# Kernel tuning notes

Measured on AMD Instinct MI355X. Metric: run time of the kernel, lower is better.

The kernel has to match this reference:

```python
import jax, jax.numpy as jnp
import numpy as np

T, H, I = 8192, 4096, 11008  # tokens, hidden, intermediate (LLaMA-7B)


def setup_inputs() -> dict:
    key = jax.random.key(0)
    ks = jax.random.split(key, 8)
    # int8-valued tensors stored as int32 (spec dtype enum lacks int8)
    hidden_states = jax.random.randint(ks[0], (T, H), -128, 128, dtype=jnp.int32)
    gate_w = jax.random.randint(ks[1], (I, H), -128, 128, dtype=jnp.int32)
    up_w = jax.random.randint(ks[2], (I, H), -128, 128, dtype=jnp.int32)
    down_w = jax.random.randint(ks[3], (H, I), -128, 128, dtype=jnp.int32)
    # per-tensor dequant scales (alpha = input_scale * weight_scale); small so
    # the SwiGLU product lands roughly in int8 range before requantization
    gate_a = jnp.float32(0.004)
    up_a = jnp.float32(0.004)
    down_a = jnp.float32(0.004)
    gate_b = jax.random.normal(ks[4], (I,), dtype=jnp.float32)
    up_b = jax.random.normal(ks[5], (I,), dtype=jnp.float32)
    down_b = jax.random.normal(ks[6], (H,), dtype=jnp.float32)
    return dict(hidden_states=hidden_states, gate_w=gate_w, gate_a=gate_a,
                gate_b=gate_b, up_w=up_w, up_a=up_a, up_b=up_b,
                down_w=down_w, down_a=down_a, down_b=down_b)


def _w8a8_linear(x_i8, w_i8, alpha, bias):
    # scale alpha and fp32 bias (W8A8BFP32OFP32Linear semantics).
    acc = jnp.matmul(x_i8.astype(jnp.int8), w_i8.astype(jnp.int8).T,
                     preferred_element_type=jnp.int32)
    return acc.astype(jnp.float32) * alpha + bias


def reference(hidden_states, gate_w, gate_a, gate_b, up_w, up_a, up_b,
              down_w, down_a, down_b):
    x1 = jax.nn.silu(_w8a8_linear(hidden_states, gate_w, gate_a, gate_b))  # [T,I]
    x2 = _w8a8_linear(hidden_states, up_w, up_a, up_b)                     # [T,I]
    x = x1 * x2
    # requantize: round, clamp to int8 range
    q = jnp.clip(jnp.round(x), -128.0, 127.0).astype(jnp.int32)
    return _w8a8_linear(q, down_w, down_a, down_b)                          # [T,H]
```

## Files before the change

### kernel.cpp

```cpp
#include <hip/hip_runtime.h>
#include <math.h>

#define T_DIM 8192
#define H_DIM 4096
#define I_DIM 11008

typedef int v4i  __attribute__((ext_vector_type(4)));
typedef int v16i __attribute__((ext_vector_type(16)));

#define MFMA8 __builtin_amdgcn_mfma_i32_32x32x32_i8

#define AS1(p) ((const __attribute__((address_space(1))) void*)(p))
#define AS3(p) ((__attribute__((address_space(3))) void*)(p))

#define WAITV(N) asm volatile("s_waitcnt vmcnt(" #N ")" ::: "memory")
#define BAR() __builtin_amdgcn_s_barrier()
#define LGKM(N) do { asm volatile("s_waitcnt lgkmcnt(" #N ")" ::: "memory"); \
                     __builtin_amdgcn_sched_barrier(0); } while (0)

#define DSRO(dst, base, off) \
  asm volatile("ds_read_b128 %0, %1 offset:%c2" : "=v"(dst) : "v"(base), "i"(off))

__device__ __forceinline__ unsigned ldsa(const char* p) {
  return (unsigned)(size_t)(const __attribute__((address_space(3))) char*)p;
}

#define STG(ldst, gsrc) \
  __builtin_amdgcn_global_load_lds(AS1(gsrc), AS3(ldst), 16, 0, 0)

__global__ void pack_shuf(const int* __restrict__ src, char* __restrict__ dst,
                          int nk32, long nchunk) {
  long c = (long)blockIdx.x * blockDim.x + threadIdx.x;
  long stride = (long)gridDim.x * blockDim.x;
  for (; c < nchunk; c += stride) {
    int lane = (int)(c & 63);
    long rk = c >> 6;
    long r32 = rk / nk32;
    int k32 = (int)(rk - r32 * nk32);
    const int4* s = (const int4*)(src + (r32 * 32 + (lane & 31)) * (long)(nk32 * 32)
                                      + (long)k32 * 32 + ((lane >> 5) << 4));
    int4 a = s[0], b = s[1], cc = s[2], d = s[3];
    int w0 = (a.x & 255) | ((a.y & 255) << 8) | ((a.z & 255) << 16) | (a.w << 24);
    int w1 = (b.x & 255) | ((b.y & 255) << 8) | ((b.z & 255) << 16) | (b.w << 24);
    int w2 = (cc.x & 255) | ((cc.y & 255) << 8) | ((cc.z & 255) << 16) | (cc.w << 24);
    int w3 = (d.x & 255) | ((d.y & 255) << 8) | ((d.z & 255) << 16) | (d.w << 24);
    ((int4*)dst)[c] = make_int4(w0, w1, w2, w3);
  }
}

__global__ __launch_bounds__(512, 1) void gemm_gateup(
    const char* __restrict__ A, const char* __restrict__ Bg, const char* __restrict__ Bu,
    const float* __restrict__ ga_p, const float* __restrict__ gb,
    const float* __restrict__ ua_p, const float* __restrict__ ub,
    char* __restrict__ Q)
{
  __shared__ char lds[131072];
  const int tid = threadIdx.x;
  const int l = tid & 63;
  const int w = tid >> 6;
  const int wm = w >> 2, wn = w & 3;
  const int li32 = l & 31, kg2 = l >> 5;

  const int q8 = 2752 / 8;
  int bid = blockIdx.x;
  int wgid = (bid & 7) * q8 + (bid >> 3);
  int st = wgid >> 3, r = wgid & 7;
  int sm = st / 43, sn = st - sm * 43;
  const int m0 = (sm * 4 + (r & 3)) * 256;
  const int n0 = (sn * 2 + (r >> 2)) * 128;

  const int NK = H_DIM / 32;
  const int NT = H_DIM / 64;

  v16i accg[4], accu[4];
#pragma unroll
  for (int i = 0; i < 4; ++i)
#pragma unroll
    for (int j = 0; j < 16; ++j) { accg[i][j] = 0; accu[i][j] = 0; }

  const int lo = l * 16;
  const char* pA0 = A  + ((size_t)((m0 >> 5) + w) * NK + 0) * 1024 + lo;
  const char* pA1 = A  + ((size_t)((m0 >> 5) + w) * NK + 1) * 1024 + lo;
  const char* pG  = Bg + ((size_t)((n0 >> 5) + (w >> 1)) * NK + (w & 1)) * 1024 + lo;
  const char* pU  = Bu + ((size_t)((n0 >> 5) + (w >> 1)) * NK + (w & 1)) * 1024 + lo;
  const int dA0 = w * 2048 + lo;
  const int dA1 = dA0 + 1024;
  const int dG  = 16384 + w * 1024 + lo;
  const int dU  = dG + 8192;

#define STAGE_GU(BO, tt)                                                  \
  do {                                                                    \
    size_t so = (size_t)(tt) * 2048;                                      \
    STG(lds + (BO) + dA0, pA0 + so);                                      \
    STG(lds + (BO) + dA1, pA1 + so);                                      \
    STG(lds + (BO) + dG,  pG  + so);                                      \
    STG(lds + (BO) + dU,  pU  + so);                                      \
  } while (0)

  const unsigned aA0L = ldsa(lds + (wm * 4 + 0) * 2048 + lo);
  const unsigned aA1L = ldsa(lds + (wm * 4 + 1) * 2048 + lo);
  const unsigned aA2L = ldsa(lds + (wm * 4 + 2) * 2048 + lo);
  const unsigned aA3L = ldsa(lds + (wm * 4 + 3) * 2048 + lo);
  const unsigned aGL  = ldsa(lds + 16384 + wn * 2048 + lo);
  const unsigned aUL  = ldsa(lds + 24576 + wn * 2048 + lo);
  const unsigned aA0H = aA0L + 65536, aA1H = aA1L + 65536;
  const unsigned aA2H = aA2L + 65536, aA3H = aA3L + 65536;
  const unsigned aGH  = aGL  + 65536, aUH  = aUL  + 65536;

  v4i E0, E1, E2, E3, Eg, Eu;
  v4i O0, O1, O2, O3, Og, Ou;

#define RD_GU(S, H, IMM)                                                  \
  do {                                                                    \
    DSRO(S##0, aA0##H, IMM); DSRO(S##1, aA1##H, IMM);                     \
    DSRO(S##2, aA2##H, IMM); DSRO(S##3, aA3##H, IMM);                     \
    DSRO(S##g, aG##H,  IMM); DSRO(S##u, aU##H,  IMM);                     \
  } while (0)

#define MM_GU(S)                                                          \
  do {                                                                    \
    __builtin_amdgcn_s_setprio(1);                                        \
    accg[0] = MFMA8(S##0, S##g, accg[0], 0, 0, 0);                        \
    accu[0] = MFMA8(S##0, S##u, accu[0], 0, 0, 0);                        \
    accg[1] = MFMA8(S##1, S##g, accg[1], 0, 0, 0);                        \
    accu[1] = MFMA8(S##1, S##u, accu[1], 0, 0, 0);                        \
    accg[2] = MFMA8(S##2, S##g, accg[2], 0, 0, 0);                        \
    accu[2] = MFMA8(S##2, S##u, accu[2], 0, 0, 0);                        \
    accg[3] = MFMA8(S##3, S##g, accg[3], 0, 0, 0);                        \
    accu[3] = MFMA8(S##3, S##u, accu[3], 0, 0, 0);                        \
    __builtin_amdgcn_s_setprio(0);                                        \
  } while (0)

  {
    STAGE_GU(0, 0);
    STAGE_GU(32768, 1);
    WAITV(4);
    BAR();
    RD_GU(E, L, 0);
  }

#define TILE_GU(t, CURH, CURI, NXTH, NXTI, SBO)                           \
  do {                                                                    \
    const int ts = ((t) + 2 < NT) ? ((t) + 2) : (NT - 1);                 \
    RD_GU(O, CURH, (CURI) + 1024);               \
    STAGE_GU(SBO, ts);                                                    \
    LGKM(6);                                       \
    MM_GU(E);                                                             \
    WAITV(4);                             \
    BAR();                                                                \
    if ((t) + 1 < NT) {                                                   \
      RD_GU(E, NXTH, NXTI);                             \
      LGKM(6);                                     \
    } else {                                                              \
      LGKM(0);                                                            \
    }                                                                     \
    MM_GU(O);                                                             \
  } while (0)

  for (int g = 0; g < NT / 4; ++g) {
    const int t = g * 4;
    TILE_GU(t + 0, L, 0,     L, 32768, 65536);
    TILE_GU(t + 1, L, 32768, H, 0,     98304);
    TILE_GU(t + 2, H, 0,     H, 32768, 0);
    TILE_GU(t + 3, H, 32768, L, 0,     32768);
  }
  WAITV(0);
#undef TILE_GU
#undef RD_GU
#undef MM_GU
#undef STAGE_GU

  const float ga = *ga_p, ua = *ua_p;
  const int col = n0 + wn * 32 + li32;
  const float gbv = gb[col], ubv = ub[col];
  const int k32q = (n0 >> 5) + wn;
  const int lanehi = ((li32 >> 4) & 1) << 5;
  const int bytelo = li32 & 15;
  const int NKQ = I_DIM / 32;
#pragma unroll
  for (int mi = 0; mi < 4; ++mi) {
    const int r32q = (m0 >> 5) + wm * 4 + mi;
    char* qbase = Q + ((size_t)(r32q * NKQ + k32q) << 10);
#pragma unroll
    for (int rq = 0; rq < 4; ++rq) {
#pragma unroll
      for (int rr = 0; rr < 4; ++rr) {
        const int rg = rq * 4 + rr;
        const int rowin = kg2 * 4 + rq * 8 + rr;
        float g = (float)accg[mi][rg] * ga + gbv;
        float u = (float)accu[mi][rg] * ua + ubv;
        float x1 = g / (1.0f + expf(-g));
        float x = rintf(x1 * u);
        x = fminf(fmaxf(x, -128.0f), 127.0f);
        qbase[((rowin | lanehi) << 4) + bytelo] = (char)(int)x;
      }
    }
  }
}

__global__ __launch_bounds__(512, 1) void gemm_down(
    const char* __restrict__ Qm, const char* __restrict__ Bd,
    const float* __restrict__ da_p, const float* __restrict__ db,
    float* __restrict__ out)
{
  __shared__ char lds[131072];
  const int tid = threadIdx.x;
  const int l = tid & 63;
  const int w = tid >> 6;
  const int wm = w >> 2, wn = w & 3;
  const int li32 = l & 31, kg2 = l >> 5;

  const int q8 = 512 / 8;
  int bid = blockIdx.x;
  int wgid = (bid & 7) * q8 + (bid >> 3);
  int st = wgid >> 3, r = wgid & 7;
  int sm = st >> 3, sn = st & 7;
  const int m0 = (sm * 4 + (r & 3)) * 256;
  const int n0 = (sn * 2 + (r >> 2)) * 256;

  const int NK = I_DIM / 32;
  const int NT = I_DIM / 64;

  v16i acc[4][2];
#pragma unroll
  for (int i = 0; i < 4; ++i)
#pragma unroll
    for (int n = 0; n < 2; ++n)
#pragma unroll
      for (int j = 0; j < 16; ++j) acc[i][n][j] = 0;

  const int lo = l * 16;
  const char* pA0 = Qm + ((size_t)((m0 >> 5) + w) * NK + 0) * 1024 + lo;
  const char* pA1 = Qm + ((size_t)((m0 >> 5) + w) * NK + 1) * 1024 + lo;
  const char* pB0 = Bd + ((size_t)((n0 >> 5) + w) * NK + 0) * 1024 + lo;
  const char* pB1 = Bd + ((size_t)((n0 >> 5) + w) * NK + 1) * 1024 + lo;
  const int dA0 = w * 2048 + lo;
  const int dA1 = dA0 + 1024;
  const int dB0 = 16384 + w * 2048 + lo;
  const int dB1 = dB0 + 1024;

#define STAGE_DN(BO, tt)                                                  \
  do {                                                                    \
    size_t so = (size_t)(tt) * 2048;                                      \
    STG(lds + (BO) + dA0, pA0 + so);                                      \
    STG(lds + (BO) + dA1, pA1 + so);                                      \
    STG(lds + (BO) + dB0, pB0 + so);                                      \
    STG(lds + (BO) + dB1, pB1 + so);                                      \
  } while (0)

  const unsigned aA0L = ldsa(lds + (wm * 4 + 0) * 2048 + lo);
  const unsigned aA1L = ldsa(lds + (wm * 4 + 1) * 2048 + lo);
  const unsigned aA2L = ldsa(lds + (wm * 4 + 2) * 2048 + lo);
  const unsigned aA3L = ldsa(lds + (wm * 4 + 3) * 2048 + lo);
  const unsigned aB0L = ldsa(lds + 16384 + (wn * 2 + 0) * 2048 + lo);
  const unsigned aB1L = ldsa(lds + 16384 + (wn * 2 + 1) * 2048 + lo);
  const unsigned aA0H = aA0L + 65536, aA1H = aA1L + 65536;
  const unsigned aA2H = aA2L + 65536, aA3H = aA3L + 65536;
  const unsigned aB0H = aB0L + 65536, aB1H = aB1L + 65536;

  v4i E0, E1, E2, E3, Eb0, Eb1;
  v4i O0, O1, O2, O3, Ob0, Ob1;

#define RD_DN(S, H, IMM)                                                  \
  do {                                                                    \
    DSRO(S##0, aA0##H, IMM);  DSRO(S##1, aA1##H, IMM);                    \
    DSRO(S##2, aA2##H, IMM);  DSRO(S##3, aA3##H, IMM);                    \
    DSRO(S##b0, aB0##H, IMM); DSRO(S##b1, aB1##H, IMM);                   \
  } while (0)

#define MM_DN(S)                                                          \
  do {                                                                    \
    __builtin_amdgcn_s_setprio(1);                                        \
    acc[0][0] = MFMA8(S##0, S##b0, acc[0][0], 0, 0, 0);                   \
    acc[0][1] = MFMA8(S##0, S##b1, acc[0][1], 0, 0, 0);                   \
    acc[1][0] = MFMA8(S##1, S##b0, acc[1][0], 0, 0, 0);                   \
    acc[1][1] = MFMA8(S##1, S##b1, acc[1][1], 0, 0, 0);                   \
    acc[2][0] = MFMA8(S##2, S##b0, acc[2][0], 0, 0, 0);                   \
    acc[2][1] = MFMA8(S##2, S##b1, acc[2][1], 0, 0, 0);                   \
    acc[3][0] = MFMA8(S##3, S##b0, acc[3][0], 0, 0, 0);                   \
    acc[3][1] = MFMA8(S##3, S##b1, acc[3][1], 0, 0, 0);                   \
    __builtin_amdgcn_s_setprio(0);                                        \
  } while (0)

  {
    STAGE_DN(0, 0);
    STAGE_DN(32768, 1);
    WAITV(4);
    BAR();
    RD_DN(E, L, 0);
  }

#define TILE_DN(t, CURH, CURI, NXTH, NXTI, SBO)                           \
  do {                                                                    \
    const int ts = ((t) + 2 < NT) ? ((t) + 2) : (NT - 1);                 \
    RD_DN(O, CURH, (CURI) + 1024);                                        \
    STAGE_DN(SBO, ts);                                                    \
    LGKM(6);                                                              \
    MM_DN(E);                                                             \
    WAITV(4);                                                             \
    BAR();                                                                \
    if ((t) + 1 < NT) {                                                   \
      RD_DN(E, NXTH, NXTI);                                               \
      LGKM(6);                                                            \
    } else {                                                              \
      LGKM(0);                                                            \
    }                                                                     \
    MM_DN(O);                                                             \
  } while (0)

  for (int g = 0; g < NT / 4; ++g) {
    const int t = g * 4;
    TILE_DN(t + 0, L, 0,     L, 32768, 65536);
    TILE_DN(t + 1, L, 32768, H, 0,     98304);
    TILE_DN(t + 2, H, 0,     H, 32768, 0);
    TILE_DN(t + 3, H, 32768, L, 0,     32768);
  }
  WAITV(0);
#undef TILE_DN
#undef RD_DN
#undef MM_DN
#undef STAGE_DN

  const float da = *da_p;
#pragma unroll
  for (int ni = 0; ni < 2; ++ni) {
    const int col = n0 + wn * 64 + ni * 32 + li32;
    const float dbv = db[col];
#pragma unroll
    for (int mi = 0; mi < 4; ++mi) {
      const int rowb = m0 + wm * 128 + mi * 32 + kg2 * 4;
#pragma unroll
      for (int rq = 0; rq < 4; ++rq) {
#pragma unroll
        for (int rr = 0; rr < 4; ++rr)
          out[(size_t)(rowb + rq * 8 + rr) * H_DIM + col] =
              (float)acc[mi][ni][rq * 4 + rr] * da + dbv;
      }
    }
  }
}

extern "C" void kernel_launch(void* const* d_in, const int* in_sizes, int n_in,
                              void* d_out, int out_size, void* d_ws, size_t ws_size,
                              hipStream_t stream) {
  const int*   hs = (const int*)d_in[0];
  const int*   gw = (const int*)d_in[1];
  const float* ga = (const float*)d_in[2];
  const float* gb = (const float*)d_in[3];
  const int*   uw = (const int*)d_in[4];
  const float* ua = (const float*)d_in[5];
  const float* ub = (const float*)d_in[6];
  const int*   dw = (const int*)d_in[7];
  const float* da = (const float*)d_in[8];
  const float* db = (const float*)d_in[9];

  char* ws   = (char*)d_ws;
  char* hidS = ws;
  char* gS   = hidS + (size_t)T_DIM * H_DIM;
  char* uS   = gS   + (size_t)I_DIM * H_DIM;
  char* dS   = uS   + (size_t)I_DIM * H_DIM;
  char* qS   = dS   + (size_t)H_DIM * I_DIM;

  pack_shuf<<<2048, 256, 0, stream>>>(hs, hidS, H_DIM / 32, (long)T_DIM * H_DIM / 16);
  pack_shuf<<<2048, 256, 0, stream>>>(gw, gS,   H_DIM / 32, (long)I_DIM * H_DIM / 16);
  pack_shuf<<<2048, 256, 0, stream>>>(uw, uS,   H_DIM / 32, (long)I_DIM * H_DIM / 16);
  pack_shuf<<<2048, 256, 0, stream>>>(dw, dS,   I_DIM / 32, (long)H_DIM * I_DIM / 16);

  gemm_gateup<<<2752, 512, 0, stream>>>(hidS, gS, uS, ga, gb, ua, ub, qS);
  gemm_down<<<512, 512, 0, stream>>>(qS, dS, da, db, (float*)d_out);
}
```

Measured before the change: 1.100 ms.

## Restructure GEMM main loops into split-stage ping-pong with per-phase barriers

```diff
diff --git a/kernel.cpp b/kernel.cpp
--- a/kernel.cpp
+++ b/kernel.cpp
@@ -80,7 +80,6 @@
 
   const int lo = l * 16;
   const char* pA0 = A  + ((size_t)((m0 >> 5) + w) * NK + 0) * 1024 + lo;
-  const char* pA1 = A  + ((size_t)((m0 >> 5) + w) * NK + 1) * 1024 + lo;
   const char* pG  = Bg + ((size_t)((n0 >> 5) + (w >> 1)) * NK + (w & 1)) * 1024 + lo;
   const char* pU  = Bu + ((size_t)((n0 >> 5) + (w >> 1)) * NK + (w & 1)) * 1024 + lo;
   const int dA0 = w * 2048 + lo;
@@ -88,13 +87,17 @@
   const int dG  = 16384 + w * 1024 + lo;
   const int dU  = dG + 8192;
 
-#define STAGE_GU(BO, tt)                                                  \
+#define STAGE_GA(BO, tt)                                                  \
   do {                                                                    \
     size_t so = (size_t)(tt) * 2048;                                      \
     STG(lds + (BO) + dA0, pA0 + so);                                      \
-    STG(lds + (BO) + dA1, pA1 + so);                                      \
-    STG(lds + (BO) + dG,  pG  + so);                                      \
-    STG(lds + (BO) + dU,  pU  + so);                                      \
+    STG(lds + (BO) + dA1, pA0 + so + 1024);                               \
+  } while (0)
+#define STAGE_GB(BO, tt)                                                  \
+  do {                                                                    \
+    size_t so = (size_t)(tt) * 2048;                                      \
+    STG(lds + (BO) + dG, pG + so);                                        \
+    STG(lds + (BO) + dU, pU + so);                                        \
   } while (0)
 
   const unsigned aA0L = ldsa(lds + (wm * 4 + 0) * 2048 + lo);
@@ -132,43 +135,45 @@
   } while (0)
 
   {
-    STAGE_GU(0, 0);
-    STAGE_GU(32768, 1);
+    STAGE_GA(0, 0);     STAGE_GB(0, 0);
+    STAGE_GA(32768, 1); STAGE_GB(32768, 1);
     WAITV(4);
     BAR();
-    RD_GU(E, L, 0);
-  }
-
-#define TILE_GU(t, CURH, CURI, NXTH, NXTI, SBO)                           \
+  }
+
+#define TILE_GU(t, CURH, CURI, SBO)                                       \
   do {                                                                    \
     const int ts = ((t) + 2 < NT) ? ((t) + 2) : (NT - 1);                 \
-    RD_GU(O, CURH, (CURI) + 1024);               \
-    STAGE_GU(SBO, ts);                                                    \
-    LGKM(6);                                       \
+                                                  \
+    RD_GU(E, CURH, CURI);                                                 \
+    STAGE_GA(SBO, ts);                                                    \
+    BAR();                                                                \
+    LGKM(0);                                                              \
     MM_GU(E);                                                             \
-    WAITV(4);                             \
-    BAR();                                                                \
-    if ((t) + 1 < NT) {                                                   \
-      RD_GU(E, NXTH, NXTI);                             \
-      LGKM(6);                                     \
-    } else {                                                              \
-      LGKM(0);                                                            \
-    }                                                                     \
+    BAR();                                                                \
+      \
+    RD_GU(O, CURH, (CURI) + 1024);                                        \
+    STAGE_GB(SBO, ts);                                                    \
+    WAITV(4);                                                             \
+    BAR();                                                                \
+    LGKM(0);                                                              \
     MM_GU(O);                                                             \
+    BAR();                                                                \
   } while (0)
 
   for (int g = 0; g < NT / 4; ++g) {
     const int t = g * 4;
-    TILE_GU(t + 0, L, 0,     L, 32768, 65536);
-    TILE_GU(t + 1, L, 32768, H, 0,     98304);
-    TILE_GU(t + 2, H, 0,     H, 32768, 0);
-    TILE_GU(t + 3, H, 32768, L, 0,     32768);
+    TILE_GU(t + 0, L, 0,     65536);
+    TILE_GU(t + 1, L, 32768, 98304);
+    TILE_GU(t + 2, H, 0,     0);
+    TILE_GU(t + 3, H, 32768, 32768);
   }
   WAITV(0);
 #undef TILE_GU
 #undef RD_GU
 #undef MM_GU
-#undef STAGE_GU
+#undef STAGE_GA
+#undef STAGE_GB
 
   const float ga = *ga_p, ua = *ua_p;
   const int col = n0 + wn * 32 + li32;
@@ -239,11 +244,15 @@
   const int dB0 = 16384 + w * 2048 + lo;
   const int dB1 = dB0 + 1024;
 
-#define STAGE_DN(BO, tt)                                                  \
+#define STAGE_DA(BO, tt)                                                  \
   do {                                                                    \
     size_t so = (size_t)(tt) * 2048;                                      \
     STG(lds + (BO) + dA0, pA0 + so);                                      \
     STG(lds + (BO) + dA1, pA1 + so);                                      \
+  } while (0)
+#define STAGE_DB(BO, tt)                                                  \
+  do {                                                                    \
+    size_t so = (size_t)(tt) * 2048;                                      \
     STG(lds + (BO) + dB0, pB0 + so);                                      \
     STG(lds + (BO) + dB1, pB1 + so);                                      \
   } while (0)
@@ -283,43 +292,43 @@
   } while (0)
 
   {
-    STAGE_DN(0, 0);
-    STAGE_DN(32768, 1);
+    STAGE_DA(0, 0);     STAGE_DB(0, 0);
+    STAGE_DA(32768, 1); STAGE_DB(32768, 1);
     WAITV(4);
     BAR();
-    RD_DN(E, L, 0);
-  }
-
-#define TILE_DN(t, CURH, CURI, NXTH, NXTI, SBO)                           \
+  }
+
+#define TILE_DN(t, CURH, CURI, SBO)                                       \
   do {                                                                    \
     const int ts = ((t) + 2 < NT) ? ((t) + 2) : (NT - 1);                 \
+    RD_DN(E, CURH, CURI);                                                 \
+    STAGE_DA(SBO, ts);                                                    \
+    BAR();                                                                \
+    LGKM(0);                                                              \
+    MM_DN(E);                                                             \
+    BAR();                                                                \
     RD_DN(O, CURH, (CURI) + 1024);                                        \
-    STAGE_DN(SBO, ts);                                                    \
-    LGKM(6);                                                              \
-    MM_DN(E);                                                             \
+    STAGE_DB(SBO, ts);                                                    \
     WAITV(4);                                                             \
     BAR();                                                                \
-    if ((t) + 1 < NT) {                                                   \
-      RD_DN(E, NXTH, NXTI);                                               \
-      LGKM(6);                                                            \
-    } else {                                                              \
-      LGKM(0);                                                            \
-    }                                                                     \
+    LGKM(0);                                                              \
     MM_DN(O);                                                             \
+    BAR();                                                                \
   } while (0)
 
   for (int g = 0; g < NT / 4; ++g) {
     const int t = g * 4;
-    TILE_DN(t + 0, L, 0,     L, 32768, 65536);
-    TILE_DN(t + 1, L, 32768, H, 0,     98304);
-    TILE_DN(t + 2, H, 0,     H, 32768, 0);
-    TILE_DN(t + 3, H, 32768, L, 0,     32768);
+    TILE_DN(t + 0, L, 0,     65536);
+    TILE_DN(t + 1, L, 32768, 98304);
+    TILE_DN(t + 2, H, 0,     0);
+    TILE_DN(t + 3, H, 32768, 32768);
   }
   WAITV(0);
 #undef TILE_DN
 #undef RD_DN
 #undef MM_DN
-#undef STAGE_DN
+#undef STAGE_DA
+#undef STAGE_DB
 
   const float da = *da_p;
 #pragma unroll
```

Measured after the change: 1.114 ms. No clear change (+1.3%).
